# Kernel optimization log

Hardware: AMD Instinct MI355X
Metric: run time of the kernel (lower is better)

## Reference

```python
import jax, jax.numpy as jnp
import numpy as np

NS, NM, NR, H = 5000, 100000, 2000, 128
E_SM, E_RM, E_SIM, L = 2_000_000, 1_000_000, 2_000_000, 500_000
NUM_LAYERS = 4  # flattened: layer-0 sage convs 0..3, layer-1 sage convs 0..3 -> stacked [2,4,...]


def _seg_sum(x, idx, n):
    return jax.ops.segment_sum(x, idx, num_segments=n)


def sage_conv(x_src, x_dst, Wl, bl, Wr, src, dst, n_dst):
    # PyG SAGEConv: mean-aggregate neighbor features, lin_l (with bias), + lin_r(root, no bias)
    agg = _seg_sum(x_src[src], dst, n_dst)                      # [n_dst, H]
    cnt = _seg_sum(jnp.ones_like(src, dtype=x_src.dtype), dst, n_dst)
    mean = agg / jnp.maximum(cnt, 1.0)[:, None]
    return mean @ Wl + bl + x_dst @ Wr


def gcn_conv(x, W, b, src, dst, n):
    # PyG GCNConv: add self loops, symmetric normalization deg^-1/2 (deg over dst incl. self loops)
    loop = jnp.arange(n, dtype=src.dtype)
    src2 = jnp.concatenate([src, loop])
    dst2 = jnp.concatenate([dst, loop])
    deg = _seg_sum(jnp.ones_like(dst2, dtype=x.dtype), dst2, n)
    dinv = jnp.where(deg > 0, jax.lax.rsqrt(deg), 0.0)
    norm = dinv[src2] * dinv[dst2]                               # [E+n]
    xw = x @ W                                                   # [n, H]
    out = _seg_sum(xw[src2] * norm[:, None], dst2, n)
    return out + b


def setup_inputs() -> dict:
    key = jax.random.key(0)
    ks = jax.random.split(key, 20)
    s = 0.05
    inp = {
        "emb_srna": jax.random.normal(ks[0], (NS, H), jnp.float32) * s,
        "emb_mrna": jax.random.normal(ks[1], (NM, H), jnp.float32) * s,
        "emb_rbp": jax.random.normal(ks[2], (NR, H), jnp.float32) * s,
        # stacked SAGE params: [layer=2, rel=4, ...]; rel order:
        # 0: srna->mrna, 1: mrna->srna (rev), 2: rbp->mrna, 3: mrna->rbp (rev)
        "sage_Wl": jax.random.normal(ks[3], (2, 4, H, H), jnp.float32) * s,
        "sage_bl": jnp.zeros((2, 4, H), jnp.float32),
        "sage_Wr": jax.random.normal(ks[4], (2, 4, H, H), jnp.float32) * s,
        # stacked GCN params: [layer=2, rel=2 (sim, rev_sim), ...]
        "gcn_W": jax.random.normal(ks[5], (2, 2, H, H), jnp.float32) * s,
        "gcn_b": jnp.zeros((2, 2, H), jnp.float32),
        "src_sm": jax.random.randint(ks[6], (E_SM,), 0, NS),
        "dst_sm": jax.random.randint(ks[7], (E_SM,), 0, NM),
        "src_rm": jax.random.randint(ks[8], (E_RM,), 0, NR),
        "dst_rm": jax.random.randint(ks[9], (E_RM,), 0, NM),
        "src_sim": jax.random.randint(ks[10], (E_SIM,), 0, NM),
        "dst_sim": jax.random.randint(ks[11], (E_SIM,), 0, NM),
        "lbl_srna": jax.random.randint(ks[12], (L,), 0, NS),
        "lbl_mrna": jax.random.randint(ks[13], (L,), 0, NM),
        "lbl_rbp": jax.random.randint(ks[14], (L,), 0, NR),
    }
    return inp


def reference(emb_srna, emb_mrna, emb_rbp, sage_Wl, sage_bl, sage_Wr, gcn_W, gcn_b,
              src_sm, dst_sm, src_rm, dst_rm, src_sim, dst_sim,
              lbl_srna, lbl_mrna, lbl_rbp):
    x_s, x_m, x_r = emb_srna, emb_mrna, emb_rbp
    for l in range(2):
        m_new = (
            sage_conv(x_s, x_m, sage_Wl[l, 0], sage_bl[l, 0], sage_Wr[l, 0], src_sm, dst_sm, NM)
            + sage_conv(x_r, x_m, sage_Wl[l, 2], sage_bl[l, 2], sage_Wr[l, 2], src_rm, dst_rm, NM)
            + gcn_conv(x_m, gcn_W[l, 0], gcn_b[l, 0], src_sim, dst_sim, NM)
            + gcn_conv(x_m, gcn_W[l, 1], gcn_b[l, 1], dst_sim, src_sim, NM)
        )
        s_new = sage_conv(x_m, x_s, sage_Wl[l, 1], sage_bl[l, 1], sage_Wr[l, 1], dst_sm, src_sm, NS)
        r_new = sage_conv(x_m, x_r, sage_Wl[l, 3], sage_bl[l, 3], sage_Wr[l, 3], dst_rm, src_rm, NR)
        x_s, x_m, x_r = jax.nn.relu(s_new), jax.nn.relu(m_new), jax.nn.relu(r_new)
    feat_m = x_m[lbl_mrna]
    pred_srna_mrna = jnp.sum(x_s[lbl_srna] * feat_m, axis=-1)
    pred_rbp_mrna = jnp.sum(x_r[lbl_rbp] * feat_m, axis=-1)
    return (pred_srna_mrna, pred_rbp_mrna)
```

## Files before the change

kernel.cpp:

```cpp
#include <hip/hip_runtime.h>
#include <hip/hip_bf16.h>

#define NSN 5000
#define NMN 100000
#define NRN 2000
#define HDIM 128
#define ESM 2000000
#define ERM 1000000
#define ESIM 2000000
#define LBL 500000

#define CNT_TOTAL (4 * NMN + NSN + NRN)
#define POOL_TOTAL (2 * ESM + 2 * ERM + 2 * ESIM)
#define NBTOT 1222
#define WCAP 14336
#define MAXNODES 512
#define MBLK 25000

typedef short bf16x8 __attribute__((ext_vector_type(8)));
typedef float f32x4 __attribute__((ext_vector_type(4)));

__device__ __forceinline__ unsigned short f2bf(float f) {
  unsigned u = __float_as_uint(f);
  unsigned r = (u + 0x7fffu + ((u >> 16) & 1u)) >> 16;
  return (unsigned short)r;
}
__device__ __forceinline__ float bf_lo(unsigned v) { return __uint_as_float(v << 16); }
__device__ __forceinline__ float bf_hi(unsigned v) { return __uint_as_float(v & 0xffff0000u); }
__device__ __forceinline__ unsigned pack2(float x, float y) {
  return (unsigned)f2bf(x) | ((unsigned)f2bf(y) << 16);
}
__device__ __forceinline__ void unpack8(uint4 v, float* f) {
  f[0] = bf_lo(v.x); f[1] = bf_hi(v.x);
  f[2] = bf_lo(v.y); f[3] = bf_hi(v.y);
  f[4] = bf_lo(v.z); f[5] = bf_hi(v.z);
  f[6] = bf_lo(v.w); f[7] = bf_hi(v.w);
}


__global__ void zero_int(int* __restrict__ p, int n) {
  int i = blockIdx.x * blockDim.x + threadIdx.x;
  if (i < n) p[i] = 0;
}

struct BInfo { int g; int ns; int ne; };
__device__ __forceinline__ BInfo binfo(int id) {
  BInfo bi;
  if (id < 196)       { int k = id;        bi.g = 0;                   bi.ns = k << 9; bi.ne = min(bi.ns + 512, NMN); }
  else if (id < 509)  { int k = id - 196;  bi.g = NMN;                 bi.ns = k << 4; bi.ne = min(bi.ns + 16,  NSN); }
  else if (id < 705)  { int k = id - 509;  bi.g = NMN + NSN;           bi.ns = k << 9; bi.ne = min(bi.ns + 512, NMN); }
  else if (id < 830)  { int k = id - 705;  bi.g = 2 * NMN + NSN;       bi.ns = k << 4; bi.ne = min(bi.ns + 16,  NRN); }
  else if (id < 1026) { int k = id - 830;  bi.g = 2 * NMN + NSN + NRN; bi.ns = k << 9; bi.ne = min(bi.ns + 512, NMN); }
  else                { int k = id - 1026; bi.g = 3 * NMN + NSN + NRN; bi.ns = k << 9; bi.ne = min(bi.ns + 512, NMN); }
  return bi;
}

template <int SHF, int NBF, int SHR, int NBR>
__global__ __launch_bounds__(256) void countbuckets(
    const int* __restrict__ a, const int* __restrict__ b, int n,
    int* __restrict__ bcnt, int bb) {
  __shared__ int hist[NBF + NBR];
  int tid = threadIdx.x;
  int base = blockIdx.x * 4096;
  for (int k = tid; k < NBF + NBR; k += 256) hist[k] = 0;
  __syncthreads();
  int end = min(base + 4096, n);
  for (int idx = base + tid; idx < end; idx += 256) {
    atomicAdd(&hist[b[idx] >> SHF], 1);
    atomicAdd(&hist[NBF + (a[idx] >> SHR)], 1);
  }
  __syncthreads();
  for (int k = tid; k < NBF + NBR; k += 256) {
    int c = hist[k];
    if (c) atomicAdd(&bcnt[bb + k], c);
  }
}

__global__ void scan_buckets(const int* __restrict__ bcnt, int* __restrict__ bstart,
                             int* __restrict__ bcur, int* __restrict__ off_sentinel) {
  __shared__ int buf[256];
  int t = threadIdx.x;
  int base = 0;
  for (int c0 = 0; c0 < NBTOT; c0 += 256) {
    int v = (c0 + t < NBTOT) ? bcnt[c0 + t] : 0;
    buf[t] = v; __syncthreads();
    for (int o = 1; o < 256; o <<= 1) {
      int a = (t >= o) ? buf[t - o] : 0;
      __syncthreads();
      buf[t] += a;
      __syncthreads();
    }
    if (c0 + t < NBTOT) {
      int excl = buf[t] - v + base;
      bstart[c0 + t] = excl;
      bcur[c0 + t] = excl;
    }
    base += buf[255];
    __syncthreads();
  }
  if (t == 0) { bstart[NBTOT] = base; *off_sentinel = base; }
}

template <int SHF, int NBF, int SHR, int NBR>
__global__ __launch_bounds__(256) void multisplit(
    const int* __restrict__ a, const int* __restrict__ b, int n,
    int* __restrict__ bcur, int bb, int2* __restrict__ stage) {
  __shared__ int hist[NBF + NBR];
  __shared__ int gpos[NBF + NBR];
  int tid = threadIdx.x;
  int base = blockIdx.x * 4096;
  for (int k = tid; k < NBF + NBR; k += 256) hist[k] = 0;
  __syncthreads();
  int dv[16], sv[16];
#pragma unroll
  for (int j = 0; j < 16; j++) {
    int idx = base + j * 256 + tid;
    if (idx < n) {
      sv[j] = a[idx]; dv[j] = b[idx];
      atomicAdd(&hist[dv[j] >> SHF], 1);
      atomicAdd(&hist[NBF + (sv[j] >> SHR)], 1);
    } else {
      dv[j] = -1;
    }
  }
  __syncthreads();
  for (int k = tid; k < NBF + NBR; k += 256) {
    int c = hist[k];
    gpos[k] = c ? atomicAdd(&bcur[bb + k], c) : 0;
  }
  __syncthreads();
#pragma unroll
  for (int j = 0; j < 16; j++) {
    if (dv[j] >= 0) {
      int s1 = atomicAdd(&gpos[dv[j] >> SHF], 1);
      stage[s1] = make_int2(dv[j], sv[j]);
      int s2 = atomicAdd(&gpos[NBF + (sv[j] >> SHR)], 1);
      stage[s2] = make_int2(sv[j], dv[j]);
    }
  }
}

__global__ __launch_bounds__(256) void scatter_bucket(
    const int2* __restrict__ stage, const int* __restrict__ bstart,
    int* __restrict__ cur, int* __restrict__ off, int* __restrict__ pool) {
  __shared__ int win[WCAP];
  __shared__ int hist[MAXNODES];
  __shared__ int part[256];
  int b = blockIdx.x;
  BInfo bi = binfo(b);
  int s0 = bstart[b], s1 = bstart[b + 1];
  int sz = s1 - s0, nn = bi.ne - bi.ns;
  int t = threadIdx.x;
  for (int k = t; k < nn; k += 256) hist[k] = 0;
  __syncthreads();
  for (int k = s0 + t; k < s1; k += 256)
    atomicAdd(&hist[stage[k].x - bi.ns], 1);
  __syncthreads();
  int a0 = (2 * t < nn) ? hist[2 * t] : 0;
  int a1 = (2 * t + 1 < nn) ? hist[2 * t + 1] : 0;
  part[t] = a0 + a1;
  __syncthreads();
  for (int o = 1; o < 256; o <<= 1) {
    int a = (t >= o) ? part[t - o] : 0;
    __syncthreads();
    part[t] += a;
    __syncthreads();
  }
  int e0 = part[t] - a0 - a1;
  int e1 = e0 + a0;
  if (2 * t < nn)     { off[bi.g + bi.ns + 2 * t] = s0 + e0; hist[2 * t] = e0; }
  if (2 * t + 1 < nn) { off[bi.g + bi.ns + 2 * t + 1] = s0 + e1; hist[2 * t + 1] = e1; }
  __syncthreads();
  if (sz <= WCAP) {
    for (int k = s0 + t; k < s1; k += 256) {
      int2 pr = stage[k];
      int slot = atomicAdd(&hist[pr.x - bi.ns], 1);
      win[slot] = pr.y;
    }
    __syncthreads();
    for (int k = t; k < sz; k += 256) pool[s0 + k] = win[k];
  } else {
    for (int k = s0 + t; k < s1; k += 256) {
      int2 pr = stage[k];
      int slot = atomicAdd(&cur[bi.g + pr.x], 1);
      pool[s0 + hist[pr.x - bi.ns] + slot] = pr.y;
    }
  }
}

__global__ void compute_dinv(const int* __restrict__ off1, const int* __restrict__ off2,
                             float* __restrict__ dinv1, float* __restrict__ dinv2, int n) {
  int v = blockIdx.x * blockDim.x + threadIdx.x;
  if (v < n) {
    dinv1[v] = rsqrtf((float)(off1[v + 1] - off1[v] + 1));
    dinv2[v] = rsqrtf((float)(off2[v + 1] - off2[v] + 1));
  }
}

__global__ void trans_weights(const float* __restrict__ sWl, const float* __restrict__ sWr,
                              const float* __restrict__ gW, unsigned short* __restrict__ wt) {
  int i = blockIdx.x * blockDim.x + threadIdx.x;
  if (i >= 18 * 16384) return;
  int mat = i >> 14, l = mat / 9, slot = mat % 9;
  int idx = i & 16383, nn = idx >> 7, kk = idx & 127;
  int s_ = kk * 128 + nn;
  float v;
  if (slot < 4)      v = sWl[((l * 4 + slot) << 14) + s_];
  else if (slot < 6) v = gW[((l * 2 + (slot - 4)) << 14) + s_];
  else if (slot == 6) v = sWr[((l * 4 + 0) << 14) + s_] + sWr[((l * 4 + 2) << 14) + s_];
  else if (slot == 7) v = sWr[((l * 4 + 1) << 14) + s_];
  else                v = sWr[((l * 4 + 3) << 14) + s_];
  wt[i] = f2bf(v);
}

__global__ void prep_bias(const float* __restrict__ sbl, const float* __restrict__ gb,
                          float* __restrict__ biasM) {
  int i = threadIdx.x;
  int l = i >> 7, j = i & 127;
  biasM[i] = sbl[(l * 4 + 0) * 128 + j] + sbl[(l * 4 + 2) * 128 + j] +
             gb[(l * 2 + 0) * 128 + j] + gb[(l * 2 + 1) * 128 + j];
}

__global__ void cast_all(const float2* __restrict__ es, const float2* __restrict__ em,
                         const float2* __restrict__ er, unsigned* __restrict__ os,
                         unsigned* __restrict__ om, unsigned* __restrict__ orr) {
  int i = blockIdx.x * blockDim.x + threadIdx.x;
  if (i < NSN * 64) { float2 v = es[i]; os[i] = pack2(v.x, v.y); }
  if (i < NMN * 64) { float2 v = em[i]; om[i] = pack2(v.x, v.y); }
  if (i < NRN * 64) { float2 v = er[i]; orr[i] = pack2(v.x, v.y); }
}


__device__ __forceinline__ void gsum_plain(const unsigned* __restrict__ x,
                                           const int* __restrict__ pool, int s, int e,
                                           int q, int h, float* acc) {
  for (int i0 = s; i0 < e; i0 += 8) {
    int iA = i0 + q, iB = i0 + 4 + q;
    int uA = pool[min(iA, e - 1)], uB = pool[min(iB, e - 1)];
    uint4 a = *(const uint4*)(x + (size_t)uA * 64 + h * 4);
    uint4 b = *(const uint4*)(x + (size_t)uB * 64 + h * 4);
    float sA = (iA < e) ? 1.f : 0.f, sB = (iB < e) ? 1.f : 0.f;
    float fa[8], fb[8];
    unpack8(a, fa); unpack8(b, fb);
#pragma unroll
    for (int j = 0; j < 8; j++) acc[j] = fmaf(fa[j], sA, fmaf(fb[j], sB, acc[j]));
  }
}

__device__ __forceinline__ void gsum_gcn(const unsigned* __restrict__ x,
                                         const int* __restrict__ pool,
                                         const float* __restrict__ dinv, int s, int e,
                                         int q, int h, float* acc) {
  for (int i0 = s; i0 < e; i0 += 8) {
    int iA = i0 + q, iB = i0 + 4 + q;
    int uA = pool[min(iA, e - 1)], uB = pool[min(iB, e - 1)];
    uint4 a = *(const uint4*)(x + (size_t)uA * 64 + h * 4);
    uint4 b = *(const uint4*)(x + (size_t)uB * 64 + h * 4);
    float sA = (iA < e) ? dinv[uA] : 0.f, sB = (iB < e) ? dinv[uB] : 0.f;
    float fa[8], fb[8];
    unpack8(a, fa); unpack8(b, fb);
#pragma unroll
    for (int j = 0; j < 8; j++) acc[j] = fmaf(fa[j], sA, fmaf(fb[j], sB, acc[j]));
  }
}

__device__ __forceinline__ void wave_reduce(float* acc) {
#pragma unroll
  for (int j = 0; j < 8; j++) {
    acc[j] += __shfl_xor(acc[j], 16, 64);
    acc[j] += __shfl_xor(acc[j], 32, 64);
  }
}

__global__ __launch_bounds__(256) void agg_all(
    const unsigned* __restrict__ xs, const unsigned* __restrict__ xm,
    const unsigned* __restrict__ xr, const int* __restrict__ pool,
    const int* __restrict__ off_sm, const int* __restrict__ off_rm,
    const int* __restrict__ off_si, const int* __restrict__ off_si2,
    const int* __restrict__ off_ms, const int* __restrict__ off_mr,
    const float* __restrict__ dinv1, const float* __restrict__ dinv2,
    unsigned* __restrict__ aggA, unsigned* __restrict__ aggB,
    unsigned* __restrict__ aggC, unsigned* __restrict__ aggD,
    unsigned* __restrict__ aggS, unsigned* __restrict__ aggR) {
  __shared__ float psum[3][128];
  int b = blockIdx.x;
  int lane = threadIdx.x & 63;
  int q = lane >> 4, h = lane & 15;

  if (b < MBLK) {
    int w = b * 4 + (threadIdx.x >> 6);
    if (w >= NMN) return;
    float acc[8];
    {
      int s = off_sm[w], e = off_sm[w + 1];
#pragma unroll
      for (int j = 0; j < 8; j++) acc[j] = 0.f;
      gsum_plain(xs, pool, s, e, q, h, acc);
      wave_reduce(acc);
      if (q == 0) {
        float inv = (e > s) ? 1.0f / (float)(e - s) : 0.0f;
        uint4 o;
        o.x = pack2(acc[0] * inv, acc[1] * inv);
        o.y = pack2(acc[2] * inv, acc[3] * inv);
        o.z = pack2(acc[4] * inv, acc[5] * inv);
        o.w = pack2(acc[6] * inv, acc[7] * inv);
        *(uint4*)(aggA + (size_t)w * 64 + h * 4) = o;
      }
    }
    {
      int s = off_rm[w], e = off_rm[w + 1];
#pragma unroll
      for (int j = 0; j < 8; j++) acc[j] = 0.f;
      gsum_plain(xr, pool, s, e, q, h, acc);
      wave_reduce(acc);
      if (q == 0) {
        float inv = (e > s) ? 1.0f / (float)(e - s) : 0.0f;
        uint4 o;
        o.x = pack2(acc[0] * inv, acc[1] * inv);
        o.y = pack2(acc[2] * inv, acc[3] * inv);
        o.z = pack2(acc[4] * inv, acc[5] * inv);
        o.w = pack2(acc[6] * inv, acc[7] * inv);
        *(uint4*)(aggB + (size_t)w * 64 + h * 4) = o;
      }
    }
    {
      int s = off_si[w], e = off_si[w + 1];
#pragma unroll
      for (int j = 0; j < 8; j++) acc[j] = 0.f;
      gsum_gcn(xm, pool, dinv1, s, e, q, h, acc);
      wave_reduce(acc);
      if (q == 0) {
        float dw = dinv1[w];
        uint4 xv = *(const uint4*)(xm + (size_t)w * 64 + h * 4);
        float fx[8];
        unpack8(xv, fx);
        uint4 o;
        o.x = pack2(acc[0] * dw + fx[0] * dw * dw, acc[1] * dw + fx[1] * dw * dw);
        o.y = pack2(acc[2] * dw + fx[2] * dw * dw, acc[3] * dw + fx[3] * dw * dw);
        o.z = pack2(acc[4] * dw + fx[4] * dw * dw, acc[5] * dw + fx[5] * dw * dw);
        o.w = pack2(acc[6] * dw + fx[6] * dw * dw, acc[7] * dw + fx[7] * dw * dw);
        *(uint4*)(aggC + (size_t)w * 64 + h * 4) = o;
      }
    }
    {
      int s = off_si2[w], e = off_si2[w + 1];
#pragma unroll
      for (int j = 0; j < 8; j++) acc[j] = 0.f;
      gsum_gcn(xm, pool, dinv2, s, e, q, h, acc);
      wave_reduce(acc);
      if (q == 0) {
        float dw = dinv2[w];
        uint4 xv = *(const uint4*)(xm + (size_t)w * 64 + h * 4);
        float fx[8];
        unpack8(xv, fx);
        uint4 o;
        o.x = pack2(acc[0] * dw + fx[0] * dw * dw, acc[1] * dw + fx[1] * dw * dw);
        o.y = pack2(acc[2] * dw + fx[2] * dw * dw, acc[3] * dw + fx[3] * dw * dw);
        o.z = pack2(acc[4] * dw + fx[4] * dw * dw, acc[5] * dw + fx[5] * dw * dw);
        o.w = pack2(acc[6] * dw + fx[6] * dw * dw, acc[7] * dw + fx[7] * dw * dw);
        *(uint4*)(aggD + (size_t)w * 64 + h * 4) = o;
      }
    }
  } else {
    int node;
    const int* offp;
    unsigned* outb;
    if (b < MBLK + NSN) { node = b - MBLK; offp = off_ms; outb = aggS; }
    else                { node = b - MBLK - NSN; offp = off_mr; outb = aggR; }
    int sub = threadIdx.x >> 6;
    int s = offp[node], e = offp[node + 1];
    float acc[8];
#pragma unroll
    for (int j = 0; j < 8; j++) acc[j] = 0.f;
    for (int i0 = s + sub * 4; i0 < e; i0 += 16) {
      int idx = i0 + q;
      int u = pool[min(idx, e - 1)];
      uint4 a = *(const uint4*)(xm + (size_t)u * 64 + h * 4);
      float sc = (idx < e) ? 1.f : 0.f;
      float fa[8];
      unpack8(a, fa);
#pragma unroll
      for (int j = 0; j < 8; j++) acc[j] = fmaf(fa[j], sc, acc[j]);
    }
    wave_reduce(acc);
    if (sub && q == 0) {
#pragma unroll
      for (int j = 0; j < 8; j++) psum[sub - 1][h * 8 + j] = acc[j];
    }
    __syncthreads();
    if (sub == 0 && q == 0) {
#pragma unroll
      for (int j = 0; j < 8; j++)
        acc[j] += psum[0][h * 8 + j] + psum[1][h * 8 + j] + psum[2][h * 8 + j];
      float inv = (e > s) ? 1.0f / (float)(e - s) : 0.0f;
      uint4 o;
      o.x = pack2(acc[0] * inv, acc[1] * inv);
      o.y = pack2(acc[2] * inv, acc[3] * inv);
      o.z = pack2(acc[4] * inv, acc[5] * inv);
      o.w = pack2(acc[6] * inv, acc[7] * inv);
      *(uint4*)(outb + (size_t)node * 64 + h * 4) = o;
    }
  }
}


#define LDA 136

__global__ __launch_bounds__(256) void gemm_mfma(
    const unsigned short* __restrict__ a0, const unsigned short* __restrict__ w0,
    const unsigned short* __restrict__ a1, const unsigned short* __restrict__ w1,
    const unsigned short* __restrict__ a2, const unsigned short* __restrict__ w2,
    const unsigned short* __restrict__ a3, const unsigned short* __restrict__ w3,
    const unsigned short* __restrict__ a4, const unsigned short* __restrict__ w4,
    const float* __restrict__ bias, unsigned short* __restrict__ out, int n) {
  __shared__ __align__(16) unsigned short As[64 * LDA];
  __shared__ __align__(16) unsigned short Ws[128 * LDA];

  int tid = threadIdx.x;
  int w = tid >> 6, lane = tid & 63;
  int q = lane >> 4, c = lane & 15;
  int r0 = blockIdx.x * 64;

  const unsigned short* Ap[5] = {a0, a1, a2, a3, a4};
  const unsigned short* Wp[5] = {w0, w1, w2, w3, w4};

  float bias_v[8];
#pragma unroll
  for (int n0 = 0; n0 < 8; n0++) bias_v[n0] = bias[n0 * 16 + c];

  f32x4 acc[8];
#pragma unroll
  for (int n0 = 0; n0 < 8; n0++) acc[n0] = (f32x4){0.f, 0.f, 0.f, 0.f};

  for (int p = 0; p < 5; p++) {
    if (!Ap[p]) continue;
    __syncthreads();
    for (int j = tid; j < 2048; j += 256) {
      int row = j >> 4, colc = (j & 15) * 8;
      *(uint4*)&Ws[row * LDA + colc] = *(const uint4*)(Wp[p] + row * 128 + colc);
    }
    for (int j = tid; j < 1024; j += 256) {
      int row = j >> 4, colc = (j & 15) * 8;
      uint4 v = make_uint4(0u, 0u, 0u, 0u);
      if (r0 + row < n) v = *(const uint4*)(Ap[p] + (size_t)(r0 + row) * 128 + colc);
      *(uint4*)&As[row * LDA + colc] = v;
    }
    __syncthreads();

    int arow = (w * 16 + c) * LDA;
#pragma unroll
    for (int k0 = 0; k0 < 128; k0 += 32) {
      bf16x8 af = *(const bf16x8*)&As[arow + k0 + q * 8];
#pragma unroll
      for (int n0 = 0; n0 < 8; n0++) {
        bf16x8 bfv = *(const bf16x8*)&Ws[(n0 * 16 + c) * LDA + k0 + q * 8];
        acc[n0] = __builtin_amdgcn_mfma_f32_16x16x32_bf16(af, bfv, acc[n0], 0, 0, 0);
      }
    }
  }

  __syncthreads();
#pragma unroll
  for (int n0 = 0; n0 < 8; n0++) {
#pragma unroll
    for (int reg = 0; reg < 4; reg++) {
      float v = acc[n0][reg] + bias_v[n0];
      v = fmaxf(v, 0.f);
      As[(w * 16 + q * 4 + reg) * LDA + n0 * 16 + c] = f2bf(v);
    }
  }
  __syncthreads();
  for (int j = tid; j < 1024; j += 256) {
    int row = j >> 4, colc = (j & 15) * 8;
    if (r0 + row < n)
      *(uint4*)(out + (size_t)(r0 + row) * 128 + colc) = *(const uint4*)&As[row * LDA + colc];
  }
}


__global__ void dots_kernel(const unsigned* __restrict__ xs, const unsigned* __restrict__ xm,
                            const unsigned* __restrict__ xr, const int* __restrict__ ls,
                            const int* __restrict__ lm, const int* __restrict__ lr,
                            float* __restrict__ out) {
  int wv = (blockIdx.x * blockDim.x + threadIdx.x) >> 6;
  int lane = threadIdx.x & 63;
  int q = lane >> 4, h = lane & 15;
  int i = wv * 4 + q;
  if (i >= LBL) return;
  int im = lm[i], is = ls[i], ir = lr[i];
  uint4 mv = *(const uint4*)(xm + (size_t)im * 64 + h * 4);
  uint4 sv = *(const uint4*)(xs + (size_t)is * 64 + h * 4);
  uint4 rv = *(const uint4*)(xr + (size_t)ir * 64 + h * 4);
  float fm[8], fs[8], fr[8];
  unpack8(mv, fm); unpack8(sv, fs); unpack8(rv, fr);
  float p1 = 0.f, p2 = 0.f;
#pragma unroll
  for (int j = 0; j < 8; j++) { p1 = fmaf(fs[j], fm[j], p1); p2 = fmaf(fr[j], fm[j], p2); }
#pragma unroll
  for (int m = 1; m < 16; m <<= 1) {
    p1 += __shfl_xor(p1, m, 64);
    p2 += __shfl_xor(p2, m, 64);
  }
  if (h == 0) { out[i] = p1; out[LBL + i] = p2; }
}


extern "C" void kernel_launch(void* const* d_in, const int* in_sizes, int n_in,
                              void* d_out, int out_size, void* d_ws, size_t ws_size,
                              hipStream_t stream) {
  const float* emb_s = (const float*)d_in[0];
  const float* emb_m = (const float*)d_in[1];
  const float* emb_r = (const float*)d_in[2];
  const float* sWl = (const float*)d_in[3];
  const float* sbl = (const float*)d_in[4];
  const float* sWr = (const float*)d_in[5];
  const float* gW  = (const float*)d_in[6];
  const float* gb  = (const float*)d_in[7];
  const int* src_sm  = (const int*)d_in[8];
  const int* dst_sm  = (const int*)d_in[9];
  const int* src_rm  = (const int*)d_in[10];
  const int* dst_rm  = (const int*)d_in[11];
  const int* src_sim = (const int*)d_in[12];
  const int* dst_sim = (const int*)d_in[13];
  const int* lbl_s = (const int*)d_in[14];
  const int* lbl_m = (const int*)d_in[15];
  const int* lbl_r = (const int*)d_in[16];
  float* out = (float*)d_out;

  char* p = (char*)d_ws;
  auto alloc = [&](size_t bytes) -> char* {
    char* r = p;
    p += (bytes + 255) & ~(size_t)255;
    return r;
  };

  int* cnt_base = (int*)alloc(sizeof(int) * CNT_TOTAL);

  int* off_base = (int*)alloc(sizeof(int) * (CNT_TOTAL + 1));
  int* off_sm  = off_base;
  int* off_ms  = off_sm + NMN;
  int* off_rm  = off_ms + NSN;
  int* off_mr  = off_rm + NMN;
  int* off_si  = off_mr + NRN;
  int* off_si2 = off_si + NMN;

  int* bcnt   = (int*)alloc(sizeof(int) * 1280);
  int* bstart = (int*)alloc(sizeof(int) * 1280);
  int* bcur   = (int*)alloc(sizeof(int) * 1280);
  int* pool = (int*)alloc(sizeof(int) * POOL_TOTAL);

  float* dinv1 = (float*)alloc(sizeof(float) * NMN);
  float* dinv2 = (float*)alloc(sizeof(float) * NMN);

  unsigned* xsb = (unsigned*)alloc(sizeof(unsigned) * (size_t)NSN * 64);
  unsigned* xmb = (unsigned*)alloc(sizeof(unsigned) * (size_t)NMN * 64);
  unsigned* xrb = (unsigned*)alloc(sizeof(unsigned) * (size_t)NRN * 64);
  unsigned* xs0 = (unsigned*)alloc(sizeof(unsigned) * (size_t)NSN * 64);
  unsigned* xs1 = (unsigned*)alloc(sizeof(unsigned) * (size_t)NSN * 64);
  unsigned* xm0 = (unsigned*)alloc(sizeof(unsigned) * (size_t)NMN * 64);
  unsigned* xm1 = (unsigned*)alloc(sizeof(unsigned) * (size_t)NMN * 64);
  unsigned* xr0 = (unsigned*)alloc(sizeof(unsigned) * (size_t)NRN * 64);
  unsigned* xr1 = (unsigned*)alloc(sizeof(unsigned) * (size_t)NRN * 64);
  unsigned* aggA = (unsigned*)alloc(sizeof(unsigned) * (size_t)NMN * 64);
  unsigned* aggB = (unsigned*)alloc(sizeof(unsigned) * (size_t)NMN * 64);
  unsigned* aggC = (unsigned*)alloc(sizeof(unsigned) * (size_t)NMN * 64);
  unsigned* aggD = (unsigned*)alloc(sizeof(unsigned) * (size_t)NMN * 64);
  unsigned* aggS = (unsigned*)alloc(sizeof(unsigned) * (size_t)NSN * 64);
  unsigned* aggR = (unsigned*)alloc(sizeof(unsigned) * (size_t)NRN * 64);

  unsigned short* wt = (unsigned short*)alloc(sizeof(unsigned short) * 18 * 16384);
  float* biasM = (float*)alloc(sizeof(float) * 2 * 128);

  int2* stage = (int2*)aggA;

  auto WT = [&](int l, int slot) -> const unsigned short* {
    return wt + (((size_t)l * 9 + slot) << 14);
  };

  zero_int<<<5, 256, 0, stream>>>(bcnt, 1280);
  countbuckets<9, 196, 4, 313><<<(ESM + 4095) / 4096, 256, 0, stream>>>(
      src_sm, dst_sm, ESM, bcnt, 0);
  countbuckets<9, 196, 4, 125><<<(ERM + 4095) / 4096, 256, 0, stream>>>(
      src_rm, dst_rm, ERM, bcnt, 509);
  countbuckets<9, 196, 9, 196><<<(ESIM + 4095) / 4096, 256, 0, stream>>>(
      src_sim, dst_sim, ESIM, bcnt, 830);
  scan_buckets<<<1, 256, 0, stream>>>(bcnt, bstart, bcur, off_base + CNT_TOTAL);

  multisplit<9, 196, 4, 313><<<(ESM + 4095) / 4096, 256, 0, stream>>>(
      src_sm, dst_sm, ESM, bcur, 0, stage);
  multisplit<9, 196, 4, 125><<<(ERM + 4095) / 4096, 256, 0, stream>>>(
      src_rm, dst_rm, ERM, bcur, 509, stage);
  multisplit<9, 196, 9, 196><<<(ESIM + 4095) / 4096, 256, 0, stream>>>(
      src_sim, dst_sim, ESIM, bcur, 830, stage);
  zero_int<<<(CNT_TOTAL + 255) / 256, 256, 0, stream>>>(cnt_base, CNT_TOTAL);
  scatter_bucket<<<NBTOT, 256, 0, stream>>>(stage, bstart, cnt_base, off_base, pool);

  compute_dinv<<<(NMN + 255) / 256, 256, 0, stream>>>(off_si, off_si2, dinv1, dinv2, NMN);
  trans_weights<<<(18 * 16384 + 255) / 256, 256, 0, stream>>>(sWl, sWr, gW, wt);
  prep_bias<<<1, 256, 0, stream>>>(sbl, gb, biasM);
  cast_all<<<(NMN * 64 + 255) / 256, 256, 0, stream>>>((const float2*)emb_s, (const float2*)emb_m,
                                                       (const float2*)emb_r, xsb, xmb, xrb);

  const int AGG_GRID = MBLK + NSN + NRN;
  for (int l = 0; l < 2; ++l) {
    const unsigned* xs_c = l ? xs0 : xsb;
    const unsigned* xm_c = l ? xm0 : xmb;
    const unsigned* xr_c = l ? xr0 : xrb;
    unsigned* xs_n = l ? xs1 : xs0;
    unsigned* xm_n = l ? xm1 : xm0;
    unsigned* xr_n = l ? xr1 : xr0;

    agg_all<<<AGG_GRID, 256, 0, stream>>>(
        xs_c, xm_c, xr_c, pool, off_sm, off_rm, off_si, off_si2, off_ms, off_mr,
        dinv1, dinv2, aggA, aggB, aggC, aggD, aggS, aggR);

    gemm_mfma<<<(NMN + 63) / 64, 256, 0, stream>>>(
        (const unsigned short*)aggA, WT(l, 0), (const unsigned short*)aggB, WT(l, 2),
        (const unsigned short*)aggC, WT(l, 4), (const unsigned short*)aggD, WT(l, 5),
        (const unsigned short*)xm_c, WT(l, 6), biasM + l * 128,
        (unsigned short*)xm_n, NMN);
    gemm_mfma<<<(NSN + 63) / 64, 256, 0, stream>>>(
        (const unsigned short*)aggS, WT(l, 1), (const unsigned short*)xs_c, WT(l, 7),
        nullptr, nullptr, nullptr, nullptr, nullptr, nullptr,
        sbl + (l * 4 + 1) * 128, (unsigned short*)xs_n, NSN);
    gemm_mfma<<<(NRN + 63) / 64, 256, 0, stream>>>(
        (const unsigned short*)aggR, WT(l, 3), (const unsigned short*)xr_c, WT(l, 8),
        nullptr, nullptr, nullptr, nullptr, nullptr, nullptr,
        sbl + (l * 4 + 3) * 128, (unsigned short*)xr_n, NRN);
  }

  dots_kernel<<<(LBL * 16 + 255) / 256, 256, 0, stream>>>(xs1, xm1, xr1, lbl_s, lbl_m, lbl_r, out);
}
```

Before: 1.185 ms.

## Interleave four mRNA relation gathers in one loop and use packed float2 math

The mRNA aggregation now walks all four edge lists (sRNA, RBP, sim, rev-sim) in a single interleaved loop with separate accumulators, instead of four sequential loops each followed by a reduction. This puts more independent gather loads in flight per wave, which should hide the latency of random row accesses. Accumulation switches to float2 vectors so the compiler can emit packed FMA. The sRNA/RBP aggregation path processes two 4-edge groups per step with a stride of 32. The cost is more registers per thread, which may lower occupancy.

```diff
diff --git a/kernel.cpp b/kernel.cpp
--- a/kernel.cpp
+++ b/kernel.cpp
@@ -19,6 +19,7 @@
 
 typedef short bf16x8 __attribute__((ext_vector_type(8)));
 typedef float f32x4 __attribute__((ext_vector_type(4)));
+typedef float f32x2 __attribute__((ext_vector_type(2)));
 
 __device__ __forceinline__ unsigned short f2bf(float f) {
   unsigned u = __float_as_uint(f);
@@ -29,6 +30,12 @@
 __device__ __forceinline__ float bf_hi(unsigned v) { return __uint_as_float(v & 0xffff0000u); }
 __device__ __forceinline__ unsigned pack2(float x, float y) {
   return (unsigned)f2bf(x) | ((unsigned)f2bf(y) << 16);
+}
+__device__ __forceinline__ f32x2 up2(unsigned v) {
+  f32x2 r;
+  r.x = bf_lo(v);
+  r.y = bf_hi(v);
+  return r;
 }
 __device__ __forceinline__ void unpack8(uint4 v, float* f) {
   f[0] = bf_lo(v.x); f[1] = bf_hi(v.x);
@@ -231,45 +238,52 @@
 }
 
 
-__device__ __forceinline__ void gsum_plain(const unsigned* __restrict__ x,
-                                           const int* __restrict__ pool, int s, int e,
-                                           int q, int h, float* acc) {
-  for (int i0 = s; i0 < e; i0 += 8) {
-    int iA = i0 + q, iB = i0 + 4 + q;
-    int uA = pool[min(iA, e - 1)], uB = pool[min(iB, e - 1)];
-    uint4 a = *(const uint4*)(x + (size_t)uA * 64 + h * 4);
-    uint4 b = *(const uint4*)(x + (size_t)uB * 64 + h * 4);
-    float sA = (iA < e) ? 1.f : 0.f, sB = (iB < e) ? 1.f : 0.f;
-    float fa[8], fb[8];
-    unpack8(a, fa); unpack8(b, fb);
-#pragma unroll
-    for (int j = 0; j < 8; j++) acc[j] = fmaf(fa[j], sA, fmaf(fb[j], sB, acc[j]));
-  }
-}
-
-__device__ __forceinline__ void gsum_gcn(const unsigned* __restrict__ x,
+__device__ __forceinline__ void step_plain(const unsigned* __restrict__ xh,
+                                           const int* __restrict__ pool,
+                                           int i0, int e, int q, f32x2* acc) {
+  int iA = i0 + q, iB = i0 + 4 + q;
+  int uA = pool[min(iA, e - 1)], uB = pool[min(iB, e - 1)];
+  uint4 a = *(const uint4*)(xh + (size_t)uA * 64);
+  uint4 b = *(const uint4*)(xh + (size_t)uB * 64);
+  float sA = (iA < e) ? 1.f : 0.f, sB = (iB < e) ? 1.f : 0.f;
+  acc[0] += up2(a.x) * sA + up2(b.x) * sB;
+  acc[1] += up2(a.y) * sA + up2(b.y) * sB;
+  acc[2] += up2(a.z) * sA + up2(b.z) * sB;
+  acc[3] += up2(a.w) * sA + up2(b.w) * sB;
+}
+
+__device__ __forceinline__ void step_gcn(const unsigned* __restrict__ xh,
                                          const int* __restrict__ pool,
-                                         const float* __restrict__ dinv, int s, int e,
-                                         int q, int h, float* acc) {
-  for (int i0 = s; i0 < e; i0 += 8) {
-    int iA = i0 + q, iB = i0 + 4 + q;
-    int uA = pool[min(iA, e - 1)], uB = pool[min(iB, e - 1)];
-    uint4 a = *(const uint4*)(x + (size_t)uA * 64 + h * 4);
-    uint4 b = *(const uint4*)(x + (size_t)uB * 64 + h * 4);
-    float sA = (iA < e) ? dinv[uA] : 0.f, sB = (iB < e) ? dinv[uB] : 0.f;
-    float fa[8], fb[8];
-    unpack8(a, fa); unpack8(b, fb);
-#pragma unroll
-    for (int j = 0; j < 8; j++) acc[j] = fmaf(fa[j], sA, fmaf(fb[j], sB, acc[j]));
-  }
-}
-
-__device__ __forceinline__ void wave_reduce(float* acc) {
-#pragma unroll
-  for (int j = 0; j < 8; j++) {
-    acc[j] += __shfl_xor(acc[j], 16, 64);
-    acc[j] += __shfl_xor(acc[j], 32, 64);
-  }
+                                         const float* __restrict__ dinv,
+                                         int i0, int e, int q, f32x2* acc) {
+  int iA = i0 + q, iB = i0 + 4 + q;
+  int uA = pool[min(iA, e - 1)], uB = pool[min(iB, e - 1)];
+  uint4 a = *(const uint4*)(xh + (size_t)uA * 64);
+  uint4 b = *(const uint4*)(xh + (size_t)uB * 64);
+  float sA = (iA < e) ? dinv[uA] : 0.f, sB = (iB < e) ? dinv[uB] : 0.f;
+  acc[0] += up2(a.x) * sA + up2(b.x) * sB;
+  acc[1] += up2(a.y) * sA + up2(b.y) * sB;
+  acc[2] += up2(a.z) * sA + up2(b.z) * sB;
+  acc[3] += up2(a.w) * sA + up2(b.w) * sB;
+}
+
+__device__ __forceinline__ void qreduce(f32x2* acc) {
+#pragma unroll
+  for (int j = 0; j < 4; j++) {
+    acc[j].x += __shfl_xor(acc[j].x, 16, 64);
+    acc[j].y += __shfl_xor(acc[j].y, 16, 64);
+    acc[j].x += __shfl_xor(acc[j].x, 32, 64);
+    acc[j].y += __shfl_xor(acc[j].y, 32, 64);
+  }
+}
+
+__device__ __forceinline__ uint4 pack_scaled(const f32x2* acc, float sc) {
+  uint4 o;
+  o.x = pack2(acc[0].x * sc, acc[0].y * sc);
+  o.y = pack2(acc[1].x * sc, acc[1].y * sc);
+  o.z = pack2(acc[2].x * sc, acc[2].y * sc);
+  o.w = pack2(acc[3].x * sc, acc[3].y * sc);
+  return o;
 }
 
 __global__ __launch_bounds__(256) void agg_all(
@@ -290,76 +304,46 @@
   if (b < MBLK) {
     int w = b * 4 + (threadIdx.x >> 6);
     if (w >= NMN) return;
-    float acc[8];
-    {
-      int s = off_sm[w], e = off_sm[w + 1];
-#pragma unroll
-      for (int j = 0; j < 8; j++) acc[j] = 0.f;
-      gsum_plain(xs, pool, s, e, q, h, acc);
-      wave_reduce(acc);
-      if (q == 0) {
-        float inv = (e > s) ? 1.0f / (float)(e - s) : 0.0f;
-        uint4 o;
-        o.x = pack2(acc[0] * inv, acc[1] * inv);
-        o.y = pack2(acc[2] * inv, acc[3] * inv);
-        o.z = pack2(acc[4] * inv, acc[5] * inv);
-        o.w = pack2(acc[6] * inv, acc[7] * inv);
-        *(uint4*)(aggA + (size_t)w * 64 + h * 4) = o;
-      }
-    }
-    {
-      int s = off_rm[w], e = off_rm[w + 1];
-#pragma unroll
-      for (int j = 0; j < 8; j++) acc[j] = 0.f;
-      gsum_plain(xr, pool, s, e, q, h, acc);
-      wave_reduce(acc);
-      if (q == 0) {
-        float inv = (e > s) ? 1.0f / (float)(e - s) : 0.0f;
-        uint4 o;
-        o.x = pack2(acc[0] * inv, acc[1] * inv);
-        o.y = pack2(acc[2] * inv, acc[3] * inv);
-        o.z = pack2(acc[4] * inv, acc[5] * inv);
-        o.w = pack2(acc[6] * inv, acc[7] * inv);
-        *(uint4*)(aggB + (size_t)w * 64 + h * 4) = o;
-      }
-    }
-    {
-      int s = off_si[w], e = off_si[w + 1];
-#pragma unroll
-      for (int j = 0; j < 8; j++) acc[j] = 0.f;
-      gsum_gcn(xm, pool, dinv1, s, e, q, h, acc);
-      wave_reduce(acc);
-      if (q == 0) {
-        float dw = dinv1[w];
-        uint4 xv = *(const uint4*)(xm + (size_t)w * 64 + h * 4);
-        float fx[8];
-        unpack8(xv, fx);
-        uint4 o;
-        o.x = pack2(acc[0] * dw + fx[0] * dw * dw, acc[1] * dw + fx[1] * dw * dw);
-        o.y = pack2(acc[2] * dw + fx[2] * dw * dw, acc[3] * dw + fx[3] * dw * dw);
-        o.z = pack2(acc[4] * dw + fx[4] * dw * dw, acc[5] * dw + fx[5] * dw * dw);
-        o.w = pack2(acc[6] * dw + fx[6] * dw * dw, acc[7] * dw + fx[7] * dw * dw);
-        *(uint4*)(aggC + (size_t)w * 64 + h * 4) = o;
-      }
-    }
-    {
-      int s = off_si2[w], e = off_si2[w + 1];
-#pragma unroll
-      for (int j = 0; j < 8; j++) acc[j] = 0.f;
-      gsum_gcn(xm, pool, dinv2, s, e, q, h, acc);
-      wave_reduce(acc);
-      if (q == 0) {
-        float dw = dinv2[w];
-        uint4 xv = *(const uint4*)(xm + (size_t)w * 64 + h * 4);
-        float fx[8];
-        unpack8(xv, fx);
-        uint4 o;
-        o.x = pack2(acc[0] * dw + fx[0] * dw * dw, acc[1] * dw + fx[1] * dw * dw);
-        o.y = pack2(acc[2] * dw + fx[2] * dw * dw, acc[3] * dw + fx[3] * dw * dw);
-        o.z = pack2(acc[4] * dw + fx[4] * dw * dw, acc[5] * dw + fx[5] * dw * dw);
-        o.w = pack2(acc[6] * dw + fx[6] * dw * dw, acc[7] * dw + fx[7] * dw * dw);
-        *(uint4*)(aggD + (size_t)w * 64 + h * 4) = o;
-      }
+    const unsigned* xsh = xs + h * 4;
+    const unsigned* xmh = xm + h * 4;
+    const unsigned* xrh = xr + h * 4;
+    int iA = off_sm[w],  eA = off_sm[w + 1];
+    int iB = off_rm[w],  eB = off_rm[w + 1];
+    int iC = off_si[w],  eC = off_si[w + 1];
+    int iD = off_si2[w], eD = off_si2[w + 1];
+    int sA = iA, sB = iB, sC = iC, sD = iD;
+    f32x2 accA[4], accB[4], accC[4], accD[4];
+#pragma unroll
+    for (int j = 0; j < 4; j++) {
+      accA[j] = (f32x2)(0.f); accB[j] = (f32x2)(0.f);
+      accC[j] = (f32x2)(0.f); accD[j] = (f32x2)(0.f);
+    }
+    while ((iA < eA) | (iB < eB) | (iC < eC) | (iD < eD)) {
+      if (iA < eA) { step_plain(xsh, pool, iA, eA, q, accA); iA += 8; }
+      if (iB < eB) { step_plain(xrh, pool, iB, eB, q, accB); iB += 8; }
+      if (iC < eC) { step_gcn(xmh, pool, dinv1, iC, eC, q, accC); iC += 8; }
+      if (iD < eD) { step_gcn(xmh, pool, dinv2, iD, eD, q, accD); iD += 8; }
+    }
+    qreduce(accA); qreduce(accB); qreduce(accC); qreduce(accD);
+    if (q == 0) {
+      float invA = (eA > sA) ? 1.0f / (float)(eA - sA) : 0.0f;
+      float invB = (eB > sB) ? 1.0f / (float)(eB - sB) : 0.0f;
+      *(uint4*)(aggA + (size_t)w * 64 + h * 4) = pack_scaled(accA, invA);
+      *(uint4*)(aggB + (size_t)w * 64 + h * 4) = pack_scaled(accB, invB);
+      float d1 = dinv1[w], d2 = dinv2[w];
+      uint4 xv = *(const uint4*)(xmh + (size_t)w * 64);
+      f32x2 fx[4] = {up2(xv.x), up2(xv.y), up2(xv.z), up2(xv.w)};
+      uint4 oC, oD;
+      f32x2 c0 = accC[0] * d1 + fx[0] * (d1 * d1), c1 = accC[1] * d1 + fx[1] * (d1 * d1);
+      f32x2 c2 = accC[2] * d1 + fx[2] * (d1 * d1), c3 = accC[3] * d1 + fx[3] * (d1 * d1);
+      oC.x = pack2(c0.x, c0.y); oC.y = pack2(c1.x, c1.y);
+      oC.z = pack2(c2.x, c2.y); oC.w = pack2(c3.x, c3.y);
+      f32x2 d0v = accD[0] * d2 + fx[0] * (d2 * d2), d1v = accD[1] * d2 + fx[1] * (d2 * d2);
+      f32x2 d2v = accD[2] * d2 + fx[2] * (d2 * d2), d3v = accD[3] * d2 + fx[3] * (d2 * d2);
+      oD.x = pack2(d0v.x, d0v.y); oD.y = pack2(d1v.x, d1v.y);
+      oD.z = pack2(d2v.x, d2v.y); oD.w = pack2(d3v.x, d3v.y);
+      *(uint4*)(aggC + (size_t)w * 64 + h * 4) = oC;
+      *(uint4*)(aggD + (size_t)w * 64 + h * 4) = oD;
     }
   } else {
     int node;
@@ -367,38 +351,31 @@
     unsigned* outb;
     if (b < MBLK + NSN) { node = b - MBLK; offp = off_ms; outb = aggS; }
     else                { node = b - MBLK - NSN; offp = off_mr; outb = aggR; }
+    const unsigned* xmh = xm + h * 4;
     int sub = threadIdx.x >> 6;
     int s = offp[node], e = offp[node + 1];
-    float acc[8];
-#pragma unroll
-    for (int j = 0; j < 8; j++) acc[j] = 0.f;
-    for (int i0 = s + sub * 4; i0 < e; i0 += 16) {
-      int idx = i0 + q;
-      int u = pool[min(idx, e - 1)];
-      uint4 a = *(const uint4*)(xm + (size_t)u * 64 + h * 4);
-      float sc = (idx < e) ? 1.f : 0.f;
-      float fa[8];
-      unpack8(a, fa);
-#pragma unroll
-      for (int j = 0; j < 8; j++) acc[j] = fmaf(fa[j], sc, acc[j]);
-    }
-    wave_reduce(acc);
+    f32x2 acc[4];
+#pragma unroll
+    for (int j = 0; j < 4; j++) acc[j] = (f32x2)(0.f);
+    for (int i0 = s + sub * 8; i0 < e; i0 += 32)
+      step_plain(xmh, pool, i0, e, q, acc);
+    qreduce(acc);
     if (sub && q == 0) {
 #pragma unroll
-      for (int j = 0; j < 8; j++) psum[sub - 1][h * 8 + j] = acc[j];
+      for (int j = 0; j < 4; j++) {
+        psum[sub - 1][h * 8 + 2 * j] = acc[j].x;
+        psum[sub - 1][h * 8 + 2 * j + 1] = acc[j].y;
+      }
     }
     __syncthreads();
     if (sub == 0 && q == 0) {
 #pragma unroll
-      for (int j = 0; j < 8; j++)
-        acc[j] += psum[0][h * 8 + j] + psum[1][h * 8 + j] + psum[2][h * 8 + j];
+      for (int j = 0; j < 4; j++) {
+        acc[j].x += psum[0][h * 8 + 2 * j] + psum[1][h * 8 + 2 * j] + psum[2][h * 8 + 2 * j];
+        acc[j].y += psum[0][h * 8 + 2 * j + 1] + psum[1][h * 8 + 2 * j + 1] + psum[2][h * 8 + 2 * j + 1];
+      }
       float inv = (e > s) ? 1.0f / (float)(e - s) : 0.0f;
-      uint4 o;
-      o.x = pack2(acc[0] * inv, acc[1] * inv);
-      o.y = pack2(acc[2] * inv, acc[3] * inv);
-      o.z = pack2(acc[4] * inv, acc[5] * inv);
-      o.w = pack2(acc[6] * inv, acc[7] * inv);
-      *(uint4*)(outb + (size_t)node * 64 + h * 4) = o;
+      *(uint4*)(outb + (size_t)node * 64 + h * 4) = pack_scaled(acc, inv);
     }
   }
 }
```

Measured after the change: 1.244 ms. 4.9% more time.
